# Kernel optimization log

Measured on AMD Instinct MI355X. Metric: run time of the kernel, lower is better.

The kernel has to match this reference:

```python
import jax, jax.numpy as jnp
import numpy as np
import math

NUM_BUCKETS = 32
MAX_DISTANCE = 128
N_HEADS = 16
D_KV = 64
D_MODEL = 1024


def _relative_position_bucket(relative_position, num_buckets=NUM_BUCKETS, max_distance=MAX_DISTANCE):
    # bidirectional (encoder) variant
    num_buckets = num_buckets // 2
    relative_buckets = (relative_position > 0).astype(jnp.int32) * num_buckets
    relative_position = jnp.abs(relative_position)
    max_exact = num_buckets // 2
    is_small = relative_position < max_exact
    # avoid log(0); masked by is_small anyway
    rp = jnp.maximum(relative_position, 1).astype(jnp.float32)
    rel_if_large = max_exact + (
        jnp.log(rp / max_exact) / math.log(max_distance / max_exact) * (num_buckets - max_exact)
    ).astype(jnp.int32)
    rel_if_large = jnp.minimum(rel_if_large, num_buckets - 1)
    relative_buckets = relative_buckets + jnp.where(is_small, relative_position, rel_if_large)
    return relative_buckets


def compute_bias(rel_bias, q_len, k_len):
    context = jnp.arange(q_len, dtype=jnp.int32)[:, None]
    memory = jnp.arange(k_len, dtype=jnp.int32)[None, :]
    buckets = _relative_position_bucket(memory - context)  # [q,k]
    values = rel_bias[buckets]                              # [q,k,H]
    return jnp.transpose(values, (2, 0, 1))[None]           # [1,H,q,k]


def setup_inputs() -> dict:
    key = jax.random.key(0)
    k1, k2, k3, k4 = jax.random.split(key, 4)
    B, S = 2, 2048
    hidden_states = jax.random.normal(k1, (B, S, D_MODEL), dtype=jnp.float32)
    attention_mask = jnp.ones((B, S), dtype=jnp.int32)
    w_qkv = jax.random.normal(k2, (3 * D_MODEL, D_MODEL), dtype=jnp.float32) * 0.02
    rel_bias = jax.random.normal(k3, (NUM_BUCKETS, N_HEADS), dtype=jnp.float32)
    w_o = jax.random.normal(k4, (D_MODEL, D_MODEL), dtype=jnp.float32) * 0.02
    return {"hidden_states": hidden_states, "attention_mask": attention_mask,
            "w_qkv": w_qkv, "rel_bias": rel_bias, "w_o": w_o}


def reference(hidden_states, attention_mask, w_qkv, rel_bias, w_o):
    B, S, _ = hidden_states.shape
    n, c = N_HEADS, D_KV
    qkv = hidden_states @ w_qkv.T                      # [B,S,3*inner]
    q, k, v = jnp.split(qkv, 3, axis=-1)
    q = q.reshape(B, S, n, c)
    k = k.reshape(B, S, n, c)
    v = v.reshape(B, S, n, c)
    attn_bias = jnp.broadcast_to(compute_bias(rel_bias, S, S), (B, n, S, S))
    mask = attention_mask.reshape(B, 1, 1, S)
    mask_val = jnp.finfo(q.dtype).min
    attn_bias = jnp.where(mask == 0, mask_val, attn_bias)
    attn = jnp.einsum('binc,bjnc->bnij', q, k) + attn_bias   # no 1/sqrt(d) scale in T5
    attn = jax.nn.softmax(attn.astype(jnp.float32), axis=-1).astype(q.dtype)
    x = jnp.einsum('bnij,bjnc->binc', attn, v)
    x = x.reshape(B, S, n * c)
    return x @ w_o.T
```

## Files before the change

kernel.cpp:

```cpp
#include <hip/hip_runtime.h>
#include <stdint.h>

typedef __attribute__((ext_vector_type(4))) float f32x4;
typedef __attribute__((ext_vector_type(8))) short short8;
typedef __attribute__((ext_vector_type(4))) short short4v;
typedef __attribute__((ext_vector_type(2))) unsigned uint2v;

__device__ __forceinline__ short f2bf(float f) {
    union { float f; unsigned u; } x; x.f = f;
    return (short)((x.u + 0x7fffu + ((x.u >> 16) & 1u)) >> 16);
}

__device__ __forceinline__ unsigned cvt_pk_bf16(float lo, float hi) {
    unsigned r;
    asm("v_cvt_pk_bf16_f32 %0, %1, %2" : "=v"(r) : "v"(lo), "v"(hi));
    return r;
}

__device__ __forceinline__ float fexp2(float x) {
#if __has_builtin(__builtin_amdgcn_exp2f)
    return __builtin_amdgcn_exp2f(x);
#else
    return exp2f(x);
#endif
}

#define MFMA16(a, b, c) __builtin_amdgcn_mfma_f32_16x16x32_bf16((a), (b), (c), 0, 0, 0)

__device__ __forceinline__ void gload16(const void* g, void* l) {
    __builtin_amdgcn_global_load_lds((const __attribute__((address_space(1))) void*)g,
                                     (__attribute__((address_space(3))) void*)l, 16, 0, 0);
}

__global__ __launch_bounds__(256) void cast_all(const float* __restrict__ h,
                                                const float* __restrict__ wq,
                                                const float* __restrict__ wo,
                                                short* __restrict__ hb,
                                                short* __restrict__ wqb,
                                                short* __restrict__ wob) {
    int i = blockIdx.x * 256 + threadIdx.x;
    const float* s;
    short* d;
    int j;
    if (i < 524288) { s = h; d = hb; j = i; }
    else if (i < 917504) { s = wq; d = wqb; j = i - 524288; }
    else { s = wo; d = wob; j = i - 917504; }
    float4 a = ((const float4*)s)[j * 2];
    float4 b = ((const float4*)s)[j * 2 + 1];
    short8 o;
    o[0] = f2bf(a.x); o[1] = f2bf(a.y); o[2] = f2bf(a.z); o[3] = f2bf(a.w);
    o[4] = f2bf(b.x); o[5] = f2bf(b.y); o[6] = f2bf(b.z); o[7] = f2bf(b.w);
    ((short8*)d)[j] = o;
}

template <int OUT_BF16, int QSCALE, int VFUSE>
__global__ __launch_bounds__(512, 2) void gemm8p(const short* __restrict__ A,
                                                 const short* __restrict__ B,
                                                 void* __restrict__ Cout,
                                                 short* __restrict__ vt,
                                                 int M, int N, int K) {
    __shared__ short lds[2][4][8192];
    const int t = threadIdx.x;
    const int l = t & 63, w = t >> 6;
    const int lr = l & 15, lg = l >> 4;
    const int wr = w >> 2, wc = w & 3;
    const int m0 = blockIdx.y * 256, n0 = blockIdx.x * 256;
    const int nt = K >> 6, nh = nt << 2;

    const int sr0 = t >> 2;
    const int scc = ((t & 3) ^ ((sr0 >> 1) & 3)) * 8;
    const short* As0 = A + (size_t)(m0 + sr0) * K + scc;
    const short* As1 = A + (size_t)(m0 + sr0 + 128) * K + scc;
    const short* Bs0 = B + (size_t)(n0 + sr0) * K + scc;
    const short* Bs1 = B + (size_t)(n0 + sr0 + 128) * K + scc;
    short* ldsb = &lds[0][0][0];

    auto stageH = [&](int H) {
        int Tp = H >> 2, pos = H & 3;
        int kb = Tp * 64 + ((pos <= 1) ? 32 : 0);
        short* dst = ldsb + ((Tp & 1) * 4 + pos) * 8192 + t * 8;
        if (pos & 1) {
            gload16(As0 + kb, dst);
            gload16(As1 + kb, dst + 4096);
        } else {
            gload16(Bs0 + kb, dst);
            gload16(Bs1 + kb, dst + 4096);
        }
    };

    int aoff[8], boff[4];
    #pragma unroll
    for (int mi = 0; mi < 8; ++mi) {
        int row = wr * 128 + mi * 16 + lr;
        aoff[mi] = row * 32 + (lg ^ ((row >> 1) & 3)) * 8;
    }
    #pragma unroll
    for (int ni = 0; ni < 4; ++ni) {
        int row = wc * 64 + ni * 16 + lr;
        boff[ni] = row * 32 + (lg ^ ((row >> 1) & 3)) * 8;
    }

    f32x4 acc[8][4] = {};

    for (int H = 0; H < 7; ++H) stageH(H);
    asm volatile("s_waitcnt vmcnt(6)" ::: "memory");
    __builtin_amdgcn_s_barrier();

    for (int T = 0; T < nt; ++T) {
        const short* rbase = ldsb + (T & 1) * 32768;
        const short* B1b = rbase;
        const short* A1b = rbase + 8192;
        const short* B0b = rbase + 16384;
        const short* A0b = rbase + 24576;
        const int Hs = (T << 2) + 7;
        short8 a[4], b[4];

        #pragma unroll
        for (int i = 0; i < 4; ++i) a[i] = *(const short8*)(A1b + aoff[i]);
        #pragma unroll
        for (int i = 0; i < 4; ++i) b[i] = *(const short8*)(B1b + boff[i]);
        if (Hs < nh) stageH(Hs);
        __builtin_amdgcn_sched_barrier(0);
        __builtin_amdgcn_s_barrier();
        asm volatile("s_waitcnt lgkmcnt(0)" ::: "memory");
        __builtin_amdgcn_sched_barrier(0);
        __builtin_amdgcn_s_setprio(1);
        #pragma unroll
        for (int mi = 0; mi < 4; ++mi)
            #pragma unroll
            for (int ni = 0; ni < 4; ++ni)
                acc[mi][ni] = MFMA16(a[mi], b[ni], acc[mi][ni]);
        __builtin_amdgcn_s_setprio(0);
        __builtin_amdgcn_sched_barrier(0);
        __builtin_amdgcn_s_barrier();

        #pragma unroll
        for (int i = 0; i < 4; ++i) a[i] = *(const short8*)(A1b + aoff[4 + i]);
        if (Hs + 1 < nh) stageH(Hs + 1);
        __builtin_amdgcn_sched_barrier(0);
        __builtin_amdgcn_s_barrier();
        asm volatile("s_waitcnt lgkmcnt(0)" ::: "memory");
        __builtin_amdgcn_sched_barrier(0);
        __builtin_amdgcn_s_setprio(1);
        #pragma unroll
        for (int mi = 0; mi < 4; ++mi)
            #pragma unroll
            for (int ni = 0; ni < 4; ++ni)
                acc[4 + mi][ni] = MFMA16(a[mi], b[ni], acc[4 + mi][ni]);
        __builtin_amdgcn_s_setprio(0);
        __builtin_amdgcn_sched_barrier(0);
        __builtin_amdgcn_s_barrier();

        #pragma unroll
        for (int i = 0; i < 4; ++i) a[i] = *(const short8*)(A0b + aoff[i]);
        #pragma unroll
        for (int i = 0; i < 4; ++i) b[i] = *(const short8*)(B0b + boff[i]);
        if (Hs + 2 < nh) stageH(Hs + 2);
        __builtin_amdgcn_sched_barrier(0);
        __builtin_amdgcn_s_barrier();
        asm volatile("s_waitcnt lgkmcnt(0)" ::: "memory");
        __builtin_amdgcn_sched_barrier(0);
        __builtin_amdgcn_s_setprio(1);
        #pragma unroll
        for (int mi = 0; mi < 4; ++mi)
            #pragma unroll
            for (int ni = 0; ni < 4; ++ni)
                acc[mi][ni] = MFMA16(a[mi], b[ni], acc[mi][ni]);
        __builtin_amdgcn_s_setprio(0);
        __builtin_amdgcn_sched_barrier(0);
        __builtin_amdgcn_s_barrier();

        #pragma unroll
        for (int i = 0; i < 4; ++i) a[i] = *(const short8*)(A0b + aoff[4 + i]);
        if (Hs + 3 < nh) stageH(Hs + 3);
        __builtin_amdgcn_sched_barrier(0);
        __builtin_amdgcn_s_barrier();
        asm volatile("s_waitcnt lgkmcnt(0)" ::: "memory");
        __builtin_amdgcn_sched_barrier(0);
        __builtin_amdgcn_s_setprio(1);
        #pragma unroll
        for (int mi = 0; mi < 4; ++mi)
            #pragma unroll
            for (int ni = 0; ni < 4; ++ni)
                acc[4 + mi][ni] = MFMA16(a[mi], b[ni], acc[4 + mi][ni]);
        __builtin_amdgcn_s_setprio(0);
        if (T < nt - 2) {
            asm volatile("s_waitcnt vmcnt(6)" ::: "memory");
        } else if (T == nt - 2) {
            asm volatile("s_waitcnt vmcnt(0)" ::: "memory");
        }
        __builtin_amdgcn_sched_barrier(0);
        __builtin_amdgcn_s_barrier();
    }

    if (VFUSE && n0 >= 2048) {
        #pragma unroll
        for (int mi = 0; mi < 8; ++mi)
            #pragma unroll
            for (int ni = 0; ni < 4; ++ni) {
                int nn = n0 + wc * 64 + ni * 16 + lr;
                int h = (nn - 2048) >> 6, dd = (nn - 2048) & 63;
                int mm = m0 + wr * 128 + mi * 16 + lg * 4;
                int bb = mm >> 11, s = mm & 2047;
                short4v ov;
                #pragma unroll
                for (int rr = 0; rr < 4; ++rr) ov[rr] = f2bf(acc[mi][ni][rr]);
                *(short4v*)(vt + ((size_t)(bb * 16 + h) * 64 + dd) * 2048 + s) = ov;
            }
        return;
    }
    const float qs = (QSCALE && n0 < 1024) ? 1.4426950408889634f : 1.0f;
    #pragma unroll
    for (int mi = 0; mi < 8; ++mi)
        #pragma unroll
        for (int ni = 0; ni < 4; ++ni)
            #pragma unroll
            for (int rr = 0; rr < 4; ++rr) {
                int mm = m0 + wr * 128 + mi * 16 + lg * 4 + rr;
                int nn = n0 + wc * 64 + ni * 16 + lr;
                float v = acc[mi][ni][rr] * qs;
                if (OUT_BF16) ((short*)Cout)[(size_t)mm * N + nn] = f2bf(v);
                else ((float*)Cout)[(size_t)mm * N + nn] = v;
            }
}

template <int OUT_BF16>
__global__ __launch_bounds__(256) void gemm_bt(const short* __restrict__ A,
                                               const short* __restrict__ B,
                                               void* __restrict__ Cout,
                                               int M, int N, int K) {
    __shared__ short sA[4096];
    __shared__ short sB[4096];
    const int t = threadIdx.x;
    const int l = t & 63, w = t >> 6;
    const int lr = l & 15, lg = l >> 4;
    const int m0 = blockIdx.y * 128, n0 = blockIdx.x * 128;
    const int wm = (w >> 1) * 64, wn = (w & 1) * 64;
    const int c0 = w * 64 + l, c1 = c0 + 256;
    const short* Ap0 = A + (size_t)(m0 + (c0 >> 2)) * K + (c0 & 3) * 8;
    const short* Ap1 = A + (size_t)(m0 + (c1 >> 2)) * K + (c1 & 3) * 8;
    const short* Bp0 = B + (size_t)(n0 + (c0 >> 2)) * K + (c0 & 3) * 8;
    const short* Bp1 = B + (size_t)(n0 + (c1 >> 2)) * K + (c1 & 3) * 8;
    short* lA0 = sA + w * 512;
    short* lA1 = sA + 2048 + w * 512;
    short* lB0 = sB + w * 512;
    short* lB1 = sB + 2048 + w * 512;
    f32x4 acc[4][4] = {};
    for (int k0 = 0; k0 < K; k0 += 32) {
        gload16(Ap0 + k0, lA0);
        gload16(Ap1 + k0, lA1);
        gload16(Bp0 + k0, lB0);
        gload16(Bp1 + k0, lB1);
        __syncthreads();
        short8 af[4], bfr[4];
        #pragma unroll
        for (int m = 0; m < 4; ++m) af[m] = *(const short8*)&sA[(wm + m * 16 + lr) * 32 + lg * 8];
        #pragma unroll
        for (int n = 0; n < 4; ++n) bfr[n] = *(const short8*)&sB[(wn + n * 16 + lr) * 32 + lg * 8];
        #pragma unroll
        for (int m = 0; m < 4; ++m)
            #pragma unroll
            for (int n = 0; n < 4; ++n)
                acc[m][n] = MFMA16(af[m], bfr[n], acc[m][n]);
        __syncthreads();
    }
    #pragma unroll
    for (int m = 0; m < 4; ++m)
        #pragma unroll
        for (int n = 0; n < 4; ++n)
            #pragma unroll
            for (int r = 0; r < 4; ++r) {
                int mm = m0 + wm + m * 16 + lg * 4 + r;
                int nn = n0 + wn + n * 16 + lr;
                float v = acc[m][n][r];
                if (OUT_BF16) ((short*)Cout)[(size_t)mm * N + nn] = f2bf(v);
                else ((float*)Cout)[(size_t)mm * N + nn] = v;
            }
}

__global__ __launch_bounds__(512, 4) void attn_kernel(const short* __restrict__ qkv,
                                                      const short* __restrict__ vt,
                                                      const int* __restrict__ amask,
                                                      const float* __restrict__ rel_bias,
                                                      short* __restrict__ xout) {
    __shared__ float tbl[340];
    __shared__ short sK[4096];
    __shared__ short sV[4096];
    __shared__ short sP[8][16][72];
    __shared__ int mflags[32];
    const int t = threadIdx.x;
    const int l = t & 63, w = t >> 6;
    const int lr = l & 15, lg = l >> 4;
    const int qt = blockIdx.x, bh = blockIdx.y;
    const int b = bh >> 4, h = bh & 15;
    const int q0 = qt * 128 + w * 16;
    const float LOG2E = 1.4426950408889634f;

    if (t < 32) mflags[t] = ~0;
    if (t < 337) {
        int idx = t;
        int d = idx - 168;
        int a = d < 0 ? -d : d;
        int fb = a < 8 ? a
                 : (a < 12 ? 8 : a < 16 ? 9 : a < 23 ? 10 : a < 32 ? 11
                    : a < 46 ? 12 : a < 64 ? 13 : a < 91 ? 14 : 15);
        int bk = (d > 0 ? 16 : 0) + fb;
        tbl[idx] = rel_bias[bk * 16 + h] * LOG2E;
    }
    const float rbp = rel_bias[31 * 16 + h] * LOG2E;
    const float rbn = rel_bias[15 * 16 + h] * LOG2E;

    short8 qf[2];
    #pragma unroll
    for (int ds = 0; ds < 2; ++ds)
        qf[ds] = *(const short8*)(qkv + (size_t)(b * 2048 + q0 + lr) * 3072 + h * 64 + ds * 32 + lg * 8);

    const int4 ma = ((const int4*)(amask + b * 2048))[t];

    const int srow = t >> 3;
    const int scp = ((t & 7) ^ (srow & 7)) * 8;
    const short* kgp = qkv + (size_t)(b * 2048 + srow) * 3072 + 1024 + h * 64 + scp;
    const short* vgp = vt + ((size_t)bh * 64 + srow) * 2048 + scp;
    short* dK = sK + t * 8;
    short* dV = sV + t * 8;
    const int sw8 = (lr & 7) * 8;
    const int ibb = -q0 + lg * 4 - lr + 168;

    __syncthreads();
    int mok = ma.x & ma.y & ma.z & ma.w;
    if (mok == 0) atomicAnd(&mflags[t >> 4], 0);

    f32x4 o[4] = {};
    float mreg = -1e30f, lreg = 0.f;

    for (int kt = 0; kt < 2048; kt += 64) {
        gload16(kgp + (size_t)kt * 3072, dK);
        gload16(vgp + kt, dV);
        __syncthreads();

        f32x4 pe[4];
        #pragma unroll
        for (int ct = 0; ct < 4; ++ct) {
            f32x4 z = {};
            #pragma unroll
            for (int ds = 0; ds < 2; ++ds) {
                short8 kf = *(const short8*)&sK[(ct * 16 + lr) * 64 + ((ds * 32 + lg * 8) ^ sw8)];
                z = MFMA16(kf, qf[ds], z);
            }
            pe[ct] = z;
        }

        float cb;
        if (kt >= q0 + 106) {
            cb = rbp;
        } else if (kt + 63 <= q0 - 91) {
            cb = rbn;
        } else {
            cb = 0.f;
            const int ib = kt + ibb;
            #pragma unroll
            for (int ct = 0; ct < 4; ++ct)
                #pragma unroll
                for (int r = 0; r < 4; ++r)
                    pe[ct][r] += tbl[ib + ct * 16 + r];
        }

        float t0 = fmaxf(fmaxf(pe[0][0], pe[0][1]), fmaxf(pe[0][2], pe[0][3]));
        float t1 = fmaxf(fmaxf(pe[1][0], pe[1][1]), fmaxf(pe[1][2], pe[1][3]));
        float t2 = fmaxf(fmaxf(pe[2][0], pe[2][1]), fmaxf(pe[2][2], pe[2][3]));
        float t3 = fmaxf(fmaxf(pe[3][0], pe[3][1]), fmaxf(pe[3][2], pe[3][3]));
        float lmax = fmaxf(fmaxf(t0, t1), fmaxf(t2, t3));
        if (__any(lmax > mreg - cb + 11.5f)) {
            float rm = fmaxf(lmax, __shfl_xor(lmax, 16));
            rm = fmaxf(rm, __shfl_xor(rm, 32));
            float mnew = fmaxf(mreg, rm + cb);
            float alpha = fexp2(mreg - mnew);
            lreg *= alpha;
            #pragma unroll
            for (int dt = 0; dt < 4; ++dt)
                #pragma unroll
                for (int r = 0; r < 4; ++r)
                    o[dt][r] *= alpha;
            mreg = mnew;
        }
        const float madj = mreg - cb;
        const int tok = mflags[kt >> 6];
        float rs = 0.f;
        if (tok) {
            #pragma unroll
            for (int ct = 0; ct < 4; ++ct) {
                float p[4];
                #pragma unroll
                for (int r = 0; r < 4; ++r) {
                    float pv = fexp2(pe[ct][r] - madj);
                    p[r] = pv;
                    rs += pv;
                }
                uint2v pk;
                pk[0] = cvt_pk_bf16(p[0], p[1]);
                pk[1] = cvt_pk_bf16(p[2], p[3]);
                *(uint2v*)&sP[w][lr][ct * 16 + lg * 4] = pk;
            }
        } else {
            const int4* mp = (const int4*)(amask + b * 2048 + kt);
            #pragma unroll
            for (int ct = 0; ct < 4; ++ct) {
                int4 cm = mp[ct * 4 + lg];
                float p[4];
                #pragma unroll
                for (int r = 0; r < 4; ++r) {
                    float pv = fexp2(pe[ct][r] - madj);
                    pv = ((const int*)&cm)[r] ? pv : 0.f;
                    p[r] = pv;
                    rs += pv;
                }
                uint2v pk;
                pk[0] = cvt_pk_bf16(p[0], p[1]);
                pk[1] = cvt_pk_bf16(p[2], p[3]);
                *(uint2v*)&sP[w][lr][ct * 16 + lg * 4] = pk;
            }
        }
        lreg += rs;

        #pragma unroll
        for (int kk = 0; kk < 2; ++kk) {
            short8 pf = *(const short8*)&sP[w][lr][kk * 32 + lg * 8];
            #pragma unroll
            for (int dt = 0; dt < 4; ++dt) {
                short8 vf = *(const short8*)&sV[(dt * 16 + lr) * 64 + ((kk * 32 + lg * 8) ^ sw8)];
                o[dt] = MFMA16(vf, pf, o[dt]);
            }
        }
        __syncthreads();
    }

    float lsum = lreg + __shfl_xor(lreg, 16);
    lsum += __shfl_xor(lsum, 32);
    const float inv = 1.0f / lsum;
    #pragma unroll
    for (int dt = 0; dt < 4; ++dt) {
        short4v ov;
        #pragma unroll
        for (int r = 0; r < 4; ++r) ov[r] = f2bf(o[dt][r] * inv);
        *(short4v*)(xout + (size_t)(b * 2048 + q0 + lr) * 1024 + h * 64 + dt * 16 + lg * 4) = ov;
    }
}

extern "C" void kernel_launch(void* const* d_in, const int* in_sizes, int n_in,
                              void* d_out, int out_size, void* d_ws, size_t ws_size,
                              hipStream_t stream) {
    const float* hidden = (const float*)d_in[0];
    const int* amask = (const int*)d_in[1];
    const float* w_qkv = (const float*)d_in[2];
    const float* rel_bias = (const float*)d_in[3];
    const float* w_o = (const float*)d_in[4];
    if (ws_size < 58720256) return;
    char* ws = (char*)d_ws;
    short* hidden_bf = (short*)(ws + 0);
    short* wqkv_bf   = (short*)(ws + 8388608);
    short* wo_bf     = (short*)(ws + 14680064);
    short* qkv       = (short*)(ws + 16777216);
    short* vt        = (short*)(ws + 41943040);
    short* xbuf      = (short*)(ws + 50331648);

    cast_all<<<4096, 256, 0, stream>>>(hidden, w_qkv, w_o, hidden_bf, wqkv_bf, wo_bf);
    gemm8p<1, 1, 1><<<dim3(12, 16), 512, 0, stream>>>(hidden_bf, wqkv_bf, qkv, vt, 4096, 3072, 1024);
    attn_kernel<<<dim3(16, 32), 512, 0, stream>>>(qkv, vt, amask, rel_bias, xbuf);
    gemm_bt<0><<<dim3(8, 32), 256, 0, stream>>>(xbuf, wo_bf, d_out, 4096, 1024, 1024);
}
```

Baseline: 133.6 us.

## Double attention key tile to 128 keys per iteration

Raises the key/value tile processed per loop iteration from 64 to 128 keys. K and V each get two staging loads into shared buffers of twice the size, and the V layout changes to 128-wide rows with a modified swizzle. The bias table, mask flags and band thresholds are widened to match. This halves the number of barriers and online-softmax rescale checks, at the cost of more LDS use and registers, which may lower occupancy under launch_bounds(512,4).

```diff
diff --git a/kernel.cpp b/kernel.cpp
--- a/kernel.cpp
+++ b/kernel.cpp
@@ -283,11 +283,11 @@
                                                       const int* __restrict__ amask,
                                                       const float* __restrict__ rel_bias,
                                                       short* __restrict__ xout) {
-    __shared__ float tbl[340];
-    __shared__ short sK[4096];
-    __shared__ short sV[4096];
-    __shared__ short sP[8][16][72];
-    __shared__ int mflags[32];
+    __shared__ float tbl[468];
+    __shared__ short sK[8192];
+    __shared__ short sV[8192];
+    __shared__ short sP[8][16][136];
+    __shared__ int mflags[16];
     const int t = threadIdx.x;
     const int l = t & 63, w = t >> 6;
     const int lr = l & 15, lg = l >> 4;
@@ -296,16 +296,15 @@
     const int q0 = qt * 128 + w * 16;
     const float LOG2E = 1.4426950408889634f;
 
-    if (t < 32) mflags[t] = ~0;
-    if (t < 337) {
-        int idx = t;
-        int d = idx - 168;
+    if (t < 16) mflags[t] = ~0;
+    if (t < 466) {
+        int d = t - 233;
         int a = d < 0 ? -d : d;
         int fb = a < 8 ? a
                  : (a < 12 ? 8 : a < 16 ? 9 : a < 23 ? 10 : a < 32 ? 11
                     : a < 46 ? 12 : a < 64 ? 13 : a < 91 ? 14 : 15);
         int bk = (d > 0 ? 16 : 0) + fb;
-        tbl[idx] = rel_bias[bk * 16 + h] * LOG2E;
+        tbl[t] = rel_bias[bk * 16 + h] * LOG2E;
     }
     const float rbp = rel_bias[31 * 16 + h] * LOG2E;
     const float rbn = rel_bias[15 * 16 + h] * LOG2E;
@@ -317,30 +316,39 @@
 
     const int4 ma = ((const int4*)(amask + b * 2048))[t];
 
-    const int srow = t >> 3;
-    const int scp = ((t & 7) ^ (srow & 7)) * 8;
-    const short* kgp = qkv + (size_t)(b * 2048 + srow) * 3072 + 1024 + h * 64 + scp;
-    const short* vgp = vt + ((size_t)bh * 64 + srow) * 2048 + scp;
+    const int srowK = t >> 3;
+    const int scpK = ((t & 7) ^ (srowK & 7)) * 8;
+    const short* kgp = qkv + (size_t)(b * 2048 + srowK) * 3072 + 1024 + h * 64 + scpK;
+    const short* kgp2 = kgp + (size_t)64 * 3072;
+    const int srowV = t >> 4;
+    const int ccV = t & 15;
+    const int scpV = (((ccV & 8) | ((ccV & 7) ^ (srowV & 7)))) * 8;
+    const short* vgp = vt + ((size_t)bh * 64 + srowV) * 2048 + scpV;
+    const short* vgp2 = vgp + (size_t)32 * 2048;
     short* dK = sK + t * 8;
+    short* dK2 = sK + 4096 + t * 8;
     short* dV = sV + t * 8;
+    short* dV2 = sV + 4096 + t * 8;
     const int sw8 = (lr & 7) * 8;
-    const int ibb = -q0 + lg * 4 - lr + 168;
+    const int ibb = -q0 + lg * 4 - lr + 233;
 
     __syncthreads();
     int mok = ma.x & ma.y & ma.z & ma.w;
-    if (mok == 0) atomicAnd(&mflags[t >> 4], 0);
+    if (mok == 0) atomicAnd(&mflags[t >> 5], 0);
 
     f32x4 o[4] = {};
     float mreg = -1e30f, lreg = 0.f;
 
-    for (int kt = 0; kt < 2048; kt += 64) {
+    for (int kt = 0; kt < 2048; kt += 128) {
         gload16(kgp + (size_t)kt * 3072, dK);
+        gload16(kgp2 + (size_t)kt * 3072, dK2);
         gload16(vgp + kt, dV);
+        gload16(vgp2 + kt, dV2);
         __syncthreads();
 
-        f32x4 pe[4];
-        #pragma unroll
-        for (int ct = 0; ct < 4; ++ct) {
+        f32x4 pe[8];
+        #pragma unroll
+        for (int ct = 0; ct < 8; ++ct) {
             f32x4 z = {};
             #pragma unroll
             for (int ds = 0; ds < 2; ++ds) {
@@ -353,23 +361,28 @@
         float cb;
         if (kt >= q0 + 106) {
             cb = rbp;
-        } else if (kt + 63 <= q0 - 91) {
+        } else if (kt <= q0 - 218) {
             cb = rbn;
         } else {
             cb = 0.f;
             const int ib = kt + ibb;
             #pragma unroll
-            for (int ct = 0; ct < 4; ++ct)
+            for (int ct = 0; ct < 8; ++ct)
                 #pragma unroll
                 for (int r = 0; r < 4; ++r)
                     pe[ct][r] += tbl[ib + ct * 16 + r];
         }
 
-        float t0 = fmaxf(fmaxf(pe[0][0], pe[0][1]), fmaxf(pe[0][2], pe[0][3]));
-        float t1 = fmaxf(fmaxf(pe[1][0], pe[1][1]), fmaxf(pe[1][2], pe[1][3]));
-        float t2 = fmaxf(fmaxf(pe[2][0], pe[2][1]), fmaxf(pe[2][2], pe[2][3]));
-        float t3 = fmaxf(fmaxf(pe[3][0], pe[3][1]), fmaxf(pe[3][2], pe[3][3]));
-        float lmax = fmaxf(fmaxf(t0, t1), fmaxf(t2, t3));
+        float u0 = fmaxf(fmaxf(pe[0][0], pe[0][1]), fmaxf(pe[0][2], pe[0][3]));
+        float u1 = fmaxf(fmaxf(pe[1][0], pe[1][1]), fmaxf(pe[1][2], pe[1][3]));
+        float u2 = fmaxf(fmaxf(pe[2][0], pe[2][1]), fmaxf(pe[2][2], pe[2][3]));
+        float u3 = fmaxf(fmaxf(pe[3][0], pe[3][1]), fmaxf(pe[3][2], pe[3][3]));
+        float u4 = fmaxf(fmaxf(pe[4][0], pe[4][1]), fmaxf(pe[4][2], pe[4][3]));
+        float u5 = fmaxf(fmaxf(pe[5][0], pe[5][1]), fmaxf(pe[5][2], pe[5][3]));
+        float u6 = fmaxf(fmaxf(pe[6][0], pe[6][1]), fmaxf(pe[6][2], pe[6][3]));
+        float u7 = fmaxf(fmaxf(pe[7][0], pe[7][1]), fmaxf(pe[7][2], pe[7][3]));
+        float lmax = fmaxf(fmaxf(fmaxf(u0, u1), fmaxf(u2, u3)),
+                           fmaxf(fmaxf(u4, u5), fmaxf(u6, u7)));
         if (__any(lmax > mreg - cb + 11.5f)) {
             float rm = fmaxf(lmax, __shfl_xor(lmax, 16));
             rm = fmaxf(rm, __shfl_xor(rm, 32));
@@ -384,11 +397,11 @@
             mreg = mnew;
         }
         const float madj = mreg - cb;
-        const int tok = mflags[kt >> 6];
+        const int tok = mflags[kt >> 7];
         float rs = 0.f;
         if (tok) {
             #pragma unroll
-            for (int ct = 0; ct < 4; ++ct) {
+            for (int ct = 0; ct < 8; ++ct) {
                 float p[4];
                 #pragma unroll
                 for (int r = 0; r < 4; ++r) {
@@ -404,7 +417,7 @@
         } else {
             const int4* mp = (const int4*)(amask + b * 2048 + kt);
             #pragma unroll
-            for (int ct = 0; ct < 4; ++ct) {
+            for (int ct = 0; ct < 8; ++ct) {
                 int4 cm = mp[ct * 4 + lg];
                 float p[4];
                 #pragma unroll
@@ -423,11 +436,11 @@
         lreg += rs;
 
         #pragma unroll
-        for (int kk = 0; kk < 2; ++kk) {
+        for (int kk = 0; kk < 4; ++kk) {
             short8 pf = *(const short8*)&sP[w][lr][kk * 32 + lg * 8];
             #pragma unroll
             for (int dt = 0; dt < 4; ++dt) {
-                short8 vf = *(const short8*)&sV[(dt * 16 + lr) * 64 + ((kk * 32 + lg * 8) ^ sw8)];
+                short8 vf = *(const short8*)&sV[(dt * 16 + lr) * 128 + ((kk * 32 + lg * 8) ^ sw8)];
                 o[dt] = MFMA16(vf, pf, o[dt]);
             }
         }
```

Measured after the change: 133.9 us. No clear change (+0.2%).

## Rewrite attention with 32x32 MFMA, register-resident P and double-buffered K/V

Applied to the files above, without the earlier changes.

The attention kernel moves from 16x16x32 to 32x32x16 bf16 MFMAs, with 4 waves of 32 query rows each instead of 8 waves of 16. The softmax probabilities now stay in registers and are rearranged with v_permlane32_swap, so the shared-memory round trip through sP is gone. K/V tiles are double-buffered in LDS with explicit vmcnt waits, which lets global loads overlap compute. The costs are higher register pressure and fewer waves per block. When the mask is not all ones, the masked path now reads the mask per element from global memory.

```diff
diff --git a/kernel.cpp b/kernel.cpp
--- a/kernel.cpp
+++ b/kernel.cpp
@@ -2,9 +2,9 @@
 #include <stdint.h>
 
 typedef __attribute__((ext_vector_type(4))) float f32x4;
+typedef __attribute__((ext_vector_type(16))) float f32x16;
 typedef __attribute__((ext_vector_type(8))) short short8;
 typedef __attribute__((ext_vector_type(4))) short short4v;
-typedef __attribute__((ext_vector_type(2))) unsigned uint2v;
 
 __device__ __forceinline__ short f2bf(float f) {
     union { float f; unsigned u; } x; x.f = f;
@@ -26,6 +26,7 @@
 }
 
 #define MFMA16(a, b, c) __builtin_amdgcn_mfma_f32_16x16x32_bf16((a), (b), (c), 0, 0, 0)
+#define MFMA32(a, b, c) __builtin_amdgcn_mfma_f32_32x32x16_bf16((a), (b), (c), 0, 0, 0)
 
 __device__ __forceinline__ void gload16(const void* g, void* l) {
     __builtin_amdgcn_global_load_lds((const __attribute__((address_space(1))) void*)g,
@@ -278,28 +279,26 @@
             }
 }
 
-__global__ __launch_bounds__(512, 4) void attn_kernel(const short* __restrict__ qkv,
+__global__ __launch_bounds__(256, 2) void attn_kernel(const short* __restrict__ qkv,
                                                       const short* __restrict__ vt,
                                                       const int* __restrict__ amask,
                                                       const float* __restrict__ rel_bias,
                                                       short* __restrict__ xout) {
-    __shared__ float tbl[340];
-    __shared__ short sK[4096];
-    __shared__ short sV[4096];
-    __shared__ short sP[8][16][72];
+    __shared__ float tbl[376];
+    __shared__ short sK[2][4096];
+    __shared__ short sV[2][4096];
     __shared__ int mflags[32];
     const int t = threadIdx.x;
     const int l = t & 63, w = t >> 6;
-    const int lr = l & 15, lg = l >> 4;
+    const int ql = l & 31, hi = l >> 5;
     const int qt = blockIdx.x, bh = blockIdx.y;
     const int b = bh >> 4, h = bh & 15;
-    const int q0 = qt * 128 + w * 16;
+    const int q0 = qt * 128 + w * 32;
     const float LOG2E = 1.4426950408889634f;
 
     if (t < 32) mflags[t] = ~0;
-    if (t < 337) {
-        int idx = t;
-        int d = idx - 168;
+    for (int idx = t; idx < 369; idx += 256) {
+        int d = idx - 184;
         int a = d < 0 ? -d : d;
         int fb = a < 8 ? a
                  : (a < 12 ? 8 : a < 16 ? 9 : a < 23 ? 10 : a < 32 ? 11
@@ -310,139 +309,165 @@
     const float rbp = rel_bias[31 * 16 + h] * LOG2E;
     const float rbn = rel_bias[15 * 16 + h] * LOG2E;
 
-    short8 qf[2];
-    #pragma unroll
-    for (int ds = 0; ds < 2; ++ds)
-        qf[ds] = *(const short8*)(qkv + (size_t)(b * 2048 + q0 + lr) * 3072 + h * 64 + ds * 32 + lg * 8);
-
-    const int4 ma = ((const int4*)(amask + b * 2048))[t];
+    short8 qf[4];
+    #pragma unroll
+    for (int dc = 0; dc < 4; ++dc)
+        qf[dc] = *(const short8*)(qkv + (size_t)(b * 2048 + q0 + ql) * 3072 +
+                                  h * 64 + dc * 16 + hi * 8);
+
+    const int4* mq = (const int4*)(amask + b * 2048 + t * 8);
+    int4 ma0 = mq[0], ma1 = mq[1];
 
     const int srow = t >> 3;
     const int scp = ((t & 7) ^ (srow & 7)) * 8;
     const short* kgp = qkv + (size_t)(b * 2048 + srow) * 3072 + 1024 + h * 64 + scp;
+    const short* kgp2 = kgp + (size_t)32 * 3072;
     const short* vgp = vt + ((size_t)bh * 64 + srow) * 2048 + scp;
-    short* dK = sK + t * 8;
-    short* dV = sV + t * 8;
-    const int sw8 = (lr & 7) * 8;
-    const int ibb = -q0 + lg * 4 - lr + 168;
+    const short* vgp2 = vgp + (size_t)32 * 2048;
+    const int swq = ql & 7;
 
     __syncthreads();
-    int mok = ma.x & ma.y & ma.z & ma.w;
-    if (mok == 0) atomicAnd(&mflags[t >> 4], 0);
-
-    f32x4 o[4] = {};
+    int mok = ma0.x & ma0.y & ma0.z & ma0.w & ma1.x & ma1.y & ma1.z & ma1.w;
+    if (mok == 0) atomicAnd(&mflags[t >> 3], 0);
+    __syncthreads();
+
+    gload16(kgp, &sK[0][0] + t * 8);
+    gload16(kgp2, &sK[0][0] + 2048 + t * 8);
+    gload16(vgp, &sV[0][0] + t * 8);
+    gload16(vgp2, &sV[0][0] + 2048 + t * 8);
+
+    f32x16 o0 = {}, o1 = {};
     float mreg = -1e30f, lreg = 0.f;
 
+    auto mkfrag = [&](const f32x16& s, int base) -> short8 {
+        unsigned w0 = cvt_pk_bf16(s[base + 0], s[base + 1]);
+        unsigned w1 = cvt_pk_bf16(s[base + 2], s[base + 3]);
+        unsigned w2 = cvt_pk_bf16(s[base + 4], s[base + 5]);
+        unsigned w3 = cvt_pk_bf16(s[base + 6], s[base + 7]);
+        asm volatile("v_permlane32_swap_b32 %0, %1" : "+v"(w0), "+v"(w2));
+        asm volatile("v_permlane32_swap_b32 %0, %1" : "+v"(w1), "+v"(w3));
+        union { unsigned u[4]; short8 s8; } r;
+        r.u[0] = w0; r.u[1] = w1; r.u[2] = w2; r.u[3] = w3;
+        return r.s8;
+    };
+
     for (int kt = 0; kt < 2048; kt += 64) {
-        gload16(kgp + (size_t)kt * 3072, dK);
-        gload16(vgp + kt, dV);
-        __syncthreads();
-
-        f32x4 pe[4];
-        #pragma unroll
-        for (int ct = 0; ct < 4; ++ct) {
-            f32x4 z = {};
-            #pragma unroll
-            for (int ds = 0; ds < 2; ++ds) {
-                short8 kf = *(const short8*)&sK[(ct * 16 + lr) * 64 + ((ds * 32 + lg * 8) ^ sw8)];
-                z = MFMA16(kf, qf[ds], z);
-            }
-            pe[ct] = z;
+        const int cur = (kt >> 6) & 1;
+        if (kt + 64 < 2048) {
+            gload16(kgp + (size_t)(kt + 64) * 3072, &sK[cur ^ 1][0] + t * 8);
+            gload16(kgp2 + (size_t)(kt + 64) * 3072, &sK[cur ^ 1][0] + 2048 + t * 8);
+            gload16(vgp + kt + 64, &sV[cur ^ 1][0] + t * 8);
+            gload16(vgp2 + kt + 64, &sV[cur ^ 1][0] + 2048 + t * 8);
+            asm volatile("s_waitcnt vmcnt(4)" ::: "memory");
+        } else {
+            asm volatile("s_waitcnt vmcnt(0)" ::: "memory");
+        }
+        __builtin_amdgcn_sched_barrier(0);
+        __builtin_amdgcn_s_barrier();
+        __builtin_amdgcn_sched_barrier(0);
+
+        const short* kb = &sK[cur][0];
+        const short* vb = &sV[cur][0];
+
+        f32x16 s0 = {}, s1 = {};
+        #pragma unroll
+        for (int dc = 0; dc < 4; ++dc) {
+            short8 kf0 = *(const short8*)&kb[ql * 64 + (((dc * 2 + hi) ^ swq) * 8)];
+            short8 kf1 = *(const short8*)&kb[(32 + ql) * 64 + (((dc * 2 + hi) ^ swq) * 8)];
+            s0 = MFMA32(kf0, qf[dc], s0);
+            s1 = MFMA32(kf1, qf[dc], s1);
         }
 
         float cb;
-        if (kt >= q0 + 106) {
+        if (kt >= q0 + 122) {
             cb = rbp;
         } else if (kt + 63 <= q0 - 91) {
             cb = rbn;
         } else {
             cb = 0.f;
-            const int ib = kt + ibb;
-            #pragma unroll
-            for (int ct = 0; ct < 4; ++ct)
-                #pragma unroll
-                for (int r = 0; r < 4; ++r)
-                    pe[ct][r] += tbl[ib + ct * 16 + r];
-        }
-
-        float t0 = fmaxf(fmaxf(pe[0][0], pe[0][1]), fmaxf(pe[0][2], pe[0][3]));
-        float t1 = fmaxf(fmaxf(pe[1][0], pe[1][1]), fmaxf(pe[1][2], pe[1][3]));
-        float t2 = fmaxf(fmaxf(pe[2][0], pe[2][1]), fmaxf(pe[2][2], pe[2][3]));
-        float t3 = fmaxf(fmaxf(pe[3][0], pe[3][1]), fmaxf(pe[3][2], pe[3][3]));
-        float lmax = fmaxf(fmaxf(t0, t1), fmaxf(t2, t3));
+            const int ib = kt - q0 - ql + 184;
+            #pragma unroll
+            for (int reg = 0; reg < 16; ++reg) {
+                const int row = (reg & 3) + 8 * (reg >> 2) + 4 * hi;
+                s0[reg] += tbl[ib + row];
+                s1[reg] += tbl[ib + 32 + row];
+            }
+        }
+
+        float m0 = fmaxf(s0[0], s0[1]), m1 = fmaxf(s0[2], s0[3]);
+        float m2 = fmaxf(s0[4], s0[5]), m3 = fmaxf(s0[6], s0[7]);
+        float m4 = fmaxf(s0[8], s0[9]), m5 = fmaxf(s0[10], s0[11]);
+        float m6 = fmaxf(s0[12], s0[13]), m7 = fmaxf(s0[14], s0[15]);
+        float n0_ = fmaxf(s1[0], s1[1]), n1 = fmaxf(s1[2], s1[3]);
+        float n2 = fmaxf(s1[4], s1[5]), n3 = fmaxf(s1[6], s1[7]);
+        float n4 = fmaxf(s1[8], s1[9]), n5 = fmaxf(s1[10], s1[11]);
+        float n6 = fmaxf(s1[12], s1[13]), n7 = fmaxf(s1[14], s1[15]);
+        float lmax = fmaxf(
+            fmaxf(fmaxf(fmaxf(m0, m1), fmaxf(m2, m3)), fmaxf(fmaxf(m4, m5), fmaxf(m6, m7))),
+            fmaxf(fmaxf(fmaxf(n0_, n1), fmaxf(n2, n3)), fmaxf(fmaxf(n4, n5), fmaxf(n6, n7))));
         if (__any(lmax > mreg - cb + 11.5f)) {
-            float rm = fmaxf(lmax, __shfl_xor(lmax, 16));
-            rm = fmaxf(rm, __shfl_xor(rm, 32));
+            float rm = fmaxf(lmax, __shfl_xor(lmax, 32));
             float mnew = fmaxf(mreg, rm + cb);
             float alpha = fexp2(mreg - mnew);
             lreg *= alpha;
             #pragma unroll
-            for (int dt = 0; dt < 4; ++dt)
-                #pragma unroll
-                for (int r = 0; r < 4; ++r)
-                    o[dt][r] *= alpha;
+            for (int reg = 0; reg < 16; ++reg) {
+                o0[reg] *= alpha;
+                o1[reg] *= alpha;
+            }
             mreg = mnew;
         }
         const float madj = mreg - cb;
         const int tok = mflags[kt >> 6];
+        #pragma unroll
+        for (int reg = 0; reg < 16; ++reg) {
+            s0[reg] = fexp2(s0[reg] - madj);
+            s1[reg] = fexp2(s1[reg] - madj);
+        }
+        if (!tok) {
+            #pragma unroll
+            for (int reg = 0; reg < 16; ++reg) {
+                const int row = (reg & 3) + 8 * (reg >> 2) + 4 * hi;
+                s0[reg] = amask[b * 2048 + kt + row] ? s0[reg] : 0.f;
+                s1[reg] = amask[b * 2048 + kt + 32 + row] ? s1[reg] : 0.f;
+            }
+        }
         float rs = 0.f;
-        if (tok) {
-            #pragma unroll
-            for (int ct = 0; ct < 4; ++ct) {
-                float p[4];
-                #pragma unroll
-                for (int r = 0; r < 4; ++r) {
-                    float pv = fexp2(pe[ct][r] - madj);
-                    p[r] = pv;
-                    rs += pv;
-                }
-                uint2v pk;
-                pk[0] = cvt_pk_bf16(p[0], p[1]);
-                pk[1] = cvt_pk_bf16(p[2], p[3]);
-                *(uint2v*)&sP[w][lr][ct * 16 + lg * 4] = pk;
-            }
-        } else {
-            const int4* mp = (const int4*)(amask + b * 2048 + kt);
-            #pragma unroll
-            for (int ct = 0; ct < 4; ++ct) {
-                int4 cm = mp[ct * 4 + lg];
-                float p[4];
-                #pragma unroll
-                for (int r = 0; r < 4; ++r) {
-                    float pv = fexp2(pe[ct][r] - madj);
-                    pv = ((const int*)&cm)[r] ? pv : 0.f;
-                    p[r] = pv;
-                    rs += pv;
-                }
-                uint2v pk;
-                pk[0] = cvt_pk_bf16(p[0], p[1]);
-                pk[1] = cvt_pk_bf16(p[2], p[3]);
-                *(uint2v*)&sP[w][lr][ct * 16 + lg * 4] = pk;
-            }
-        }
+        #pragma unroll
+        for (int reg = 0; reg < 16; ++reg) rs += s0[reg] + s1[reg];
         lreg += rs;
 
-        #pragma unroll
-        for (int kk = 0; kk < 2; ++kk) {
-            short8 pf = *(const short8*)&sP[w][lr][kk * 32 + lg * 8];
-            #pragma unroll
-            for (int dt = 0; dt < 4; ++dt) {
-                short8 vf = *(const short8*)&sV[(dt * 16 + lr) * 64 + ((kk * 32 + lg * 8) ^ sw8)];
-                o[dt] = MFMA16(vf, pf, o[dt]);
-            }
-        }
-        __syncthreads();
-    }
-
-    float lsum = lreg + __shfl_xor(lreg, 16);
-    lsum += __shfl_xor(lsum, 32);
+        short8 pf0 = mkfrag(s0, 0);
+        short8 pf1 = mkfrag(s0, 8);
+        short8 pf2 = mkfrag(s1, 0);
+        short8 pf3 = mkfrag(s1, 8);
+
+        #pragma unroll
+        for (int kc = 0; kc < 4; ++kc) {
+            short8 pf = (kc == 0) ? pf0 : (kc == 1) ? pf1 : (kc == 2) ? pf2 : pf3;
+            short8 vf0 = *(const short8*)&vb[ql * 64 + (((kc * 2 + hi) ^ swq) * 8)];
+            short8 vf1 = *(const short8*)&vb[(32 + ql) * 64 + (((kc * 2 + hi) ^ swq) * 8)];
+            o0 = MFMA32(vf0, pf, o0);
+            o1 = MFMA32(vf1, pf, o1);
+        }
+        __builtin_amdgcn_sched_barrier(0);
+        __builtin_amdgcn_s_barrier();
+        __builtin_amdgcn_sched_barrier(0);
+    }
+
+    float lsum = lreg + __shfl_xor(lreg, 32);
     const float inv = 1.0f / lsum;
-    #pragma unroll
-    for (int dt = 0; dt < 4; ++dt) {
-        short4v ov;
-        #pragma unroll
-        for (int r = 0; r < 4; ++r) ov[r] = f2bf(o[dt][r] * inv);
-        *(short4v*)(xout + (size_t)(b * 2048 + q0 + lr) * 1024 + h * 64 + dt * 16 + lg * 4) = ov;
+    short* xrow = xout + (size_t)(b * 2048 + q0 + ql) * 1024 + h * 64;
+    #pragma unroll
+    for (int g = 0; g < 4; ++g) {
+        short4v ov0, ov1;
+        #pragma unroll
+        for (int r = 0; r < 4; ++r) {
+            ov0[r] = f2bf(o0[g * 4 + r] * inv);
+            ov1[r] = f2bf(o1[g * 4 + r] * inv);
+        }
+        *(short4v*)(xrow + g * 8 + 4 * hi) = ov0;
+        *(short4v*)(xrow + 32 + g * 8 + 4 * hi) = ov1;
     }
 }
 
@@ -465,6 +490,6 @@
 
     cast_all<<<4096, 256, 0, stream>>>(hidden, w_qkv, w_o, hidden_bf, wqkv_bf, wo_bf);
     gemm8p<1, 1, 1><<<dim3(12, 16), 512, 0, stream>>>(hidden_bf, wqkv_bf, qkv, vt, 4096, 3072, 1024);
-    attn_kernel<<<dim3(16, 32), 512, 0, stream>>>(qkv, vt, amask, rel_bias, xbuf);
+    attn_kernel<<<dim3(16, 32), 256, 0, stream>>>(qkv, vt, amask, rel_bias, xbuf);
     gemm_bt<0><<<dim3(8, 32), 256, 0, stream>>>(xbuf, wo_bf, d_out, 4096, 1024, 1024);
 }
```

After: 134.5 us. No clear change (+0.7%).
